# Optimization experiments

Measured on AMD Instinct MI355X. Metric: run time of the kernel, lower is better.

The kernel has to match this reference:

```python
import jax, jax.numpy as jnp
import numpy as np

B, S, D = 1, 2048, 1024
F = 1408            # expert intermediate dim
E = 16              # num experts
K = 2               # top_k
CAP_FACTOR = 1.25


def _mlp(h, wg, wu, wd):
    # DeepSeek-style gated MLP (SwiGLU, no bias)
    return (jax.nn.silu(h @ wg) * (h @ wu)) @ wd


def setup_inputs() -> dict:
    key = jax.random.key(0)
    ks = jax.random.split(key, 10)
    sd = 0.02
    return {
        "x": jax.random.normal(ks[0], (B, S, D), jnp.float32),
        "router_w": jax.random.normal(ks[1], (D, E), jnp.float32) * sd,
        "router_b": jnp.zeros((E,), jnp.float32),
        "w_gate": jax.random.normal(ks[2], (E, D, F), jnp.float32) * sd,
        "w_up": jax.random.normal(ks[3], (E, D, F), jnp.float32) * sd,
        "w_down": jax.random.normal(ks[4], (E, F, D), jnp.float32) * sd,
        "sw_gate": jax.random.normal(ks[5], (D, F), jnp.float32) * sd,
        "sw_up": jax.random.normal(ks[6], (D, F), jnp.float32) * sd,
        "sw_down": jax.random.normal(ks[7], (F, D), jnp.float32) * sd,
    }


def reference(x, router_w, router_b, w_gate, w_up, w_down, sw_gate, sw_up, sw_down):
    b, s, d = x.shape
    N = b * s
    NK = N * K
    C = int(np.ceil(CAP_FACTOR * NK / E))  # per-expert capacity

    x_tokens = x.reshape(N, d)

    # Router: softmax -> top-k -> renormalize
    logits = x_tokens @ router_w + router_b           # [N, E]
    probs = jax.nn.softmax(logits, axis=-1)
    vals, idx = jax.lax.top_k(probs, K)               # [N, K]
    vals = vals / (jnp.sum(vals, axis=-1, keepdims=True) + 1e-9)
    idx_flat = idx.reshape(NK)                        # int expert ids
    vals_flat = vals.reshape(NK)

    # Position within each expert's buffer = rank in flattened (token, k) order.
    # Same math as (cumsum(one_hot)*one_hot).sum(-1)-1 in the original.
    oh_e = jax.nn.one_hot(idx_flat, E, dtype=x.dtype)             # [NK, E] (small)
    pos = (jnp.cumsum(oh_e, axis=0) * oh_e).sum(axis=1) - 1       # [NK]
    within = (pos < C).astype(x.dtype)                            # capacity mask
    pos_c = jnp.clip(pos, 0, C - 1).astype(jnp.int32)

    # Dispatch: scatter tokens into per-expert buffers. Positions are unique
    # per expert, so scatter-add equals the dense one-hot einsum exactly.
    token_ids = jnp.arange(NK) // K
    x_pair = x_tokens[token_ids] * within[:, None]                # [NK, D]
    expert_inputs = jnp.zeros((E, C, d), x.dtype).at[idx_flat, pos_c].add(x_pair)

    # Grouped expert MLPs
    expert_outputs = jax.vmap(_mlp)(expert_inputs, w_gate, w_up, w_down)  # [E, C, D]

    # Combine: gather back and weight by renormalized router probs
    gathered = expert_outputs[idx_flat, pos_c] * (vals_flat * within)[:, None]
    output_tokens = gathered.reshape(N, K, d).sum(axis=1)         # [N, D]

    return x + _mlp(x, sw_gate, sw_up, sw_down) + output_tokens.reshape(b, s, d)
```

## Files before the change

### kernel.cpp

```cpp
#include <hip/hip_runtime.h>
#include <hip/hip_bf16.h>

#define TOKENS 2048
#define DIM    1024
#define FDIM   1408
#define NEXP   16
#define NK     (TOKENS * 2)
#define CAP    320
#define RPAD   384

typedef __attribute__((ext_vector_type(4))) float f32x4;
typedef __attribute__((ext_vector_type(8))) short s16x8;
typedef __attribute__((ext_vector_type(4))) short s16x4;

__device__ __forceinline__ short f2bf(float f) {
    unsigned int u = __float_as_uint(f);
    u += 0x7FFFu + ((u >> 16) & 1u);
    return (short)(u >> 16);
}
__device__ __forceinline__ float bf2f(short s) {
    return __uint_as_float(((unsigned int)(unsigned short)s) << 16);
}

#define GLDS16(gp, lp) __builtin_amdgcn_global_load_lds(                     \
    (const __attribute__((address_space(1))) unsigned int*)(gp),             \
    (__attribute__((address_space(3))) unsigned int*)(lp), 16, 0, 0)

struct GSeg {
    const short* A; long aStride; int aRpad;
    const short* B0; const short* B1; long bStride;
    short* Out; long oStride; int oRpad;
    const int* cnt; int Mb, Nb, N, K, nblocks;
};
struct WSeg { const float* in; short* out; int K, N, mats, nblocks; };

__device__ void wchunk_dev(const WSeg& W, int bid)
{
    const int pm  = W.nblocks / W.mats;
    const int mat = bid / pm, r = bid % pm;
    const int nbl = W.N >> 7;
    const int nb  = r % nbl, kb = r / nbl;
    const int t   = threadIdx.x;
    const int n   = nb * 128 + (t & 127);
    const int s0  = kb * 16 + (t >> 7);
    const float* in = W.in + (size_t)mat * W.K * W.N;
    short* out = W.out + (size_t)mat * W.K * W.N;
#pragma unroll
    for (int i = 0; i < 8; i++) {
        int s = s0 + i * 2;
        const float* src = in + (size_t)s * 8 * W.N + n;
        s16x8 o;
#pragma unroll
        for (int j = 0; j < 8; j++) o[j] = f2bf(src[(size_t)j * W.N]);
        *(s16x8*)(out + (size_t)s * W.N * 8 + (size_t)n * 8) = o;
    }
}

__device__ void router_dev(const float* __restrict__ x, const float* __restrict__ rw,
                           const float* __restrict__ rb, int* __restrict__ idx_flat,
                           float* __restrict__ vals_flat, int bid)
{
    __shared__ float lg[16][17];
    const int t  = threadIdx.x;
    const int tl = t >> 4;
    const int e  = t & 15;
    const int token = bid * 16 + tl;
    const float* xr = x + (size_t)token * DIM;

    float acc = 0.f;
    for (int d4 = 0; d4 < DIM / 4; d4++) {
        float4 xv = *(const float4*)(xr + d4 * 4);
        acc += xv.x * rw[(d4 * 4 + 0) * NEXP + e];
        acc += xv.y * rw[(d4 * 4 + 1) * NEXP + e];
        acc += xv.z * rw[(d4 * 4 + 2) * NEXP + e];
        acc += xv.w * rw[(d4 * 4 + 3) * NEXP + e];
    }
    lg[tl][e] = acc + rb[e];
    __syncthreads();

    if (t < 16) {
        float l[16];
#pragma unroll
        for (int j = 0; j < 16; j++) l[j] = lg[t][j];
        float m = l[0];
#pragma unroll
        for (int j = 1; j < 16; j++) m = fmaxf(m, l[j]);
        float p[16], den = 0.f;
#pragma unroll
        for (int j = 0; j < 16; j++) { p[j] = __expf(l[j] - m); den += p[j]; }
        int i1 = -1; float b1 = -1e30f;
#pragma unroll
        for (int j = 0; j < 16; j++) if (p[j] > b1) { b1 = p[j]; i1 = j; }
        int i2 = -1; float b2 = -1e30f;
#pragma unroll
        for (int j = 0; j < 16; j++) if (j != i1 && p[j] > b2) { b2 = p[j]; i2 = j; }
        float v1 = b1 / den, v2 = b2 / den;
        float s = v1 + v2 + 1e-9f;
        int tok = bid * 16 + t;
        idx_flat[tok * 2 + 0] = i1;
        idx_flat[tok * 2 + 1] = i2;
        vals_flat[tok * 2 + 0] = v1 / s;
        vals_flat[tok * 2 + 1] = v2 / s;
    }
}

__device__ void xconv_dev(const float* __restrict__ x, short* __restrict__ xb, int bid)
{
    const int token = bid * 2 + (threadIdx.x >> 7);
    const int c = threadIdx.x & 127;
    const float* src = x + (size_t)token * DIM + c * 8;
    float4 v0 = *(const float4*)(src);
    float4 v1 = *(const float4*)(src + 4);
    s16x8 o;
    o[0] = f2bf(v0.x); o[1] = f2bf(v0.y); o[2] = f2bf(v0.z); o[3] = f2bf(v0.w);
    o[4] = f2bf(v1.x); o[5] = f2bf(v1.y); o[6] = f2bf(v1.z); o[7] = f2bf(v1.w);
    *(s16x8*)(xb + (size_t)c * (TOKENS * 8) + (size_t)token * 8) = o;
}

__global__ __launch_bounds__(256) void prep_kernel(
    WSeg w0, WSeg w1, WSeg w2, WSeg w3,
    const float* __restrict__ x, const float* __restrict__ rw,
    const float* __restrict__ rb, int* __restrict__ idx_flat,
    float* __restrict__ vals, short* __restrict__ xb)
{
    int bid = blockIdx.x;
    if (bid < w0.nblocks) { wchunk_dev(w0, bid); return; }
    bid -= w0.nblocks;
    if (bid < w1.nblocks) { wchunk_dev(w1, bid); return; }
    bid -= w1.nblocks;
    if (bid < w2.nblocks) { wchunk_dev(w2, bid); return; }
    bid -= w2.nblocks;
    if (bid < w3.nblocks) { wchunk_dev(w3, bid); return; }
    bid -= w3.nblocks;
    if (bid < TOKENS / 16) { router_dev(x, rw, rb, idx_flat, vals, bid); return; }
    bid -= TOKENS / 16;
    xconv_dev(x, xb, bid);
}

__global__ void scan_kernel(const int* __restrict__ idx_flat,
                            const float* __restrict__ vals,
                            int* __restrict__ dst, float* __restrict__ wgt,
                            int* __restrict__ cnt)
{
    const int lane = threadIdx.x;
    int base[16];
#pragma unroll
    for (int e = 0; e < 16; e++) base[e] = 0;

    for (int c = 0; c < NK / 64; c++) {
        int i = c * 64 + lane;
        int e = idx_flat[i];
        unsigned long long m[16];
#pragma unroll
        for (int ee = 0; ee < 16; ee++) m[ee] = __ballot(e == ee);
        unsigned long long mym = 0ULL; int myb = 0;
#pragma unroll
        for (int ee = 0; ee < 16; ee++) {
            bool sel = (e == ee);
            mym = sel ? m[ee] : mym;
            myb = sel ? base[ee] : myb;
        }
        int pos = myb + (int)__popcll(mym & ((1ULL << lane) - 1ULL));
        bool within = pos < CAP;
        dst[i] = within ? (e * RPAD + pos) : -1;
        wgt[i] = within ? vals[i] : 0.f;
#pragma unroll
        for (int ee = 0; ee < 16; ee++) base[ee] += (int)__popcll(m[ee]);
    }
    if (lane < 16) cnt[lane] = base[lane] < CAP ? base[lane] : CAP;
}

__global__ __launch_bounds__(256) void scatter_kernel(
    const float* __restrict__ x, const int* __restrict__ dst,
    const int* __restrict__ idx_flat, short* __restrict__ ex)
{
    const int i = blockIdx.x * 2 + (threadIdx.x >> 7);
    const int d0 = dst[i];
    if (d0 < 0) return;
    const int e = idx_flat[i];
    const int pos = d0 - e * RPAD;
    const int token = i >> 1;
    const int c = threadIdx.x & 127;
    const float* src = x + (size_t)token * DIM + c * 8;
    float4 v0 = *(const float4*)(src);
    float4 v1 = *(const float4*)(src + 4);
    s16x8 o;
    o[0] = f2bf(v0.x); o[1] = f2bf(v0.y); o[2] = f2bf(v0.z); o[3] = f2bf(v0.w);
    o[4] = f2bf(v1.x); o[5] = f2bf(v1.y); o[6] = f2bf(v1.z); o[7] = f2bf(v1.w);
    *(s16x8*)(ex + (size_t)e * (DIM * RPAD) + (size_t)c * (RPAD * 8) +
              (size_t)pos * 8) = o;
}

template <int NMAT>
__device__ void gemm_dev(const GSeg& S, int bid)
{
    constexpr int BUFS = 4096 * (1 + NMAT);
    __shared__ short lds[2 * BUFS];

    const int cpx = S.nblocks >> 3;
    const int lid = (bid & 7) * cpx + (bid >> 3);
    const int mb  = lid % S.Mb;
    const int t1  = lid / S.Mb;
    const int nb  = t1 % S.Nb;
    const int g   = t1 / S.Nb;
    const int m0 = mb * 128, n0 = nb * 128;
    if (S.cnt != nullptr && m0 >= S.cnt[g]) return;

    const int tid = threadIdx.x, lane = tid & 63, w = tid >> 6;
    const int wr = w >> 1, wc = w & 1, ln = lane & 15, kg = lane >> 4;

    const int N = S.N, K = S.K;
    const short* Ag  = S.A  + (size_t)g * S.aStride + (size_t)m0 * 8;
    const short* Bg0 = S.B0 + (size_t)g * S.bStride + (size_t)n0 * 8;
    const short* Bg1 = nullptr;
    if constexpr (NMAT == 2) Bg1 = S.B1 + (size_t)g * S.bStride + (size_t)n0 * 8;

    const size_t aR8 = (size_t)S.aRpad * 8;
    const size_t n8  = (size_t)N * 8;

    const int srow = tid & 127, sslab = tid >> 7;
    const short* aS0 = Ag  + sslab * aR8 + srow * 8;
    const short* aS1 = Ag  + (2 + sslab) * aR8 + srow * 8;
    const short* bS00 = Bg0 + sslab * n8 + srow * 8;
    const short* bS01 = Bg0 + (2 + sslab) * n8 + srow * 8;
    const short* bS10 = nullptr, *bS11 = nullptr;
    if constexpr (NMAT == 2) {
        bS10 = Bg1 + sslab * n8 + srow * 8;
        bS11 = Bg1 + (2 + sslab) * n8 + srow * 8;
    }

    const int dA0 = w * 512, dA1 = 2048 + w * 512;

    auto STG = [&](int buf, int ks) {
        const size_t ka = (size_t)ks * 4 * aR8;
        const size_t kb = (size_t)ks * 4 * n8;
        short* base = lds + buf * BUFS;
        GLDS16(aS0 + ka,  base + dA0);
        GLDS16(aS1 + ka,  base + dA1);
        GLDS16(bS00 + kb, base + 4096 + dA0);
        GLDS16(bS01 + kb, base + 4096 + dA1);
        if constexpr (NMAT == 2) {
            GLDS16(bS10 + kb, base + 8192 + dA0);
            GLDS16(bS11 + kb, base + 8192 + dA1);
        }
    };

    const int aO = kg * 1024 + (wr * 64 + ln) * 8;
    const int bO = kg * 1024 + (wc * 64 + ln) * 8;

    f32x4 acc[NMAT][4][4] = {};

    const int nt = K / 32;
    STG(0, 0); STG(1, 1);
    int cur = 0;
    for (int ks = 0; ks < nt; ks++) {
        if (ks + 1 < nt) {
            if constexpr (NMAT == 2) asm volatile("s_waitcnt vmcnt(6)" ::: "memory");
            else                     asm volatile("s_waitcnt vmcnt(4)" ::: "memory");
        } else {
            asm volatile("s_waitcnt vmcnt(0)" ::: "memory");
        }
        __builtin_amdgcn_s_barrier();
        __builtin_amdgcn_sched_barrier(0);

        const short* base = lds + cur * BUFS;
        s16x8 af[4];
#pragma unroll
        for (int m = 0; m < 4; m++)
            af[m] = *(const s16x8*)(base + aO + m * 128);
        s16x8 bf[NMAT][4];
#pragma unroll
        for (int mat = 0; mat < NMAT; mat++)
#pragma unroll
            for (int nf = 0; nf < 4; nf++)
                bf[mat][nf] = *(const s16x8*)(base + 4096 + mat * 4096 + bO + nf * 128);

        __builtin_amdgcn_s_setprio(1);
#pragma unroll
        for (int nf = 0; nf < 4; nf++)
#pragma unroll
            for (int m = 0; m < 4; m++)
#pragma unroll
                for (int mat = 0; mat < NMAT; mat++)
                    acc[mat][m][nf] = __builtin_amdgcn_mfma_f32_16x16x32_bf16(
                        af[m], bf[mat][nf], acc[mat][m][nf], 0, 0, 0);
        __builtin_amdgcn_s_setprio(0);
        __builtin_amdgcn_sched_barrier(0);
        __builtin_amdgcn_s_barrier();

        if (ks + 2 < nt) STG(cur, ks + 2);
        cur ^= 1;
    }

#pragma unroll
    for (int m = 0; m < 4; m++) {
#pragma unroll
        for (int nf = 0; nf < 4; nf++) {
            const int row = m0 + wr * 64 + m * 16 + kg * 4;
            const int col = n0 + wc * 64 + nf * 16 + ln;
#pragma unroll
            for (int j = 0; j < 4; j++) {
                if constexpr (NMAT == 2) {
                    float gv = acc[0][m][nf][j];
                    float uv = acc[1][m][nf][j];
                    float v = gv / (1.f + __expf(-gv)) * uv;
                    S.Out[(size_t)g * S.oStride + (size_t)(col >> 3) * (S.oRpad * 8) +
                          (size_t)(row + j) * 8 + (col & 7)] = f2bf(v);
                } else {
                    S.Out[(size_t)g * S.oStride + (size_t)(row + j) * N + col] =
                        f2bf(acc[0][m][nf][j]);
                }
            }
        }
    }
}

__global__ __launch_bounds__(256, 2) void gateup_kernel(GSeg s0, GSeg s1,
                                                        WSeg w0, WSeg w1)
{
    int bid = blockIdx.x;
    if (bid < s0.nblocks) { gemm_dev<2>(s0, bid); return; }
    bid -= s0.nblocks;
    if (bid < s1.nblocks) { gemm_dev<2>(s1, bid); return; }
    bid -= s1.nblocks;
    if (bid < w0.nblocks) { wchunk_dev(w0, bid); return; }
    bid -= w0.nblocks;
    wchunk_dev(w1, bid);
}

__global__ __launch_bounds__(256, 2) void down_kernel(GSeg s0, GSeg s1)
{
    int bid = blockIdx.x;
    if (bid < s0.nblocks) { gemm_dev<1>(s0, bid); return; }
    bid -= s0.nblocks;
    gemm_dev<1>(s1, bid);
}

__global__ __launch_bounds__(256) void combine_kernel(
    const float* __restrict__ x, const short* __restrict__ shout,
    const short* __restrict__ eout, const int* __restrict__ dst,
    const float* __restrict__ wgt, float* __restrict__ out)
{
    const int t = blockIdx.x;
    const int d = threadIdx.x * 4;
    size_t o = (size_t)t * DIM + d;
    float4 xv = *(const float4*)(x + o);
    s16x4 sv = *(const s16x4*)(shout + o);
    float r0 = xv.x + bf2f(sv[0]);
    float r1 = xv.y + bf2f(sv[1]);
    float r2 = xv.z + bf2f(sv[2]);
    float r3 = xv.w + bf2f(sv[3]);
#pragma unroll
    for (int k = 0; k < 2; k++) {
        int di = dst[t * 2 + k];
        if (di >= 0) {
            float wv = wgt[t * 2 + k];
            s16x4 ev = *(const s16x4*)(eout + (size_t)di * DIM + d);
            r0 += wv * bf2f(ev[0]);
            r1 += wv * bf2f(ev[1]);
            r2 += wv * bf2f(ev[2]);
            r3 += wv * bf2f(ev[3]);
        }
    }
    float4 rv = {r0, r1, r2, r3};
    *(float4*)(out + o) = rv;
}

extern "C" void kernel_launch(void* const* d_in, const int* in_sizes, int n_in,
                              void* d_out, int out_size, void* d_ws, size_t ws_size,
                              hipStream_t stream)
{
    const float* x   = (const float*)d_in[0];
    const float* rw  = (const float*)d_in[1];
    const float* rb  = (const float*)d_in[2];
    const float* wg  = (const float*)d_in[3];
    const float* wu  = (const float*)d_in[4];
    const float* wd  = (const float*)d_in[5];
    const float* swg = (const float*)d_in[6];
    const float* swu = (const float*)d_in[7];
    const float* swd = (const float*)d_in[8];
    float* out = (float*)d_out;

    char* wp = (char*)d_ws;
    auto alloc = [&](size_t b) { char* p = wp; wp += (b + 255) & ~(size_t)255; return p; };
    int*   idx_flat = (int*)alloc((size_t)NK * 4);
    float* vals     = (float*)alloc((size_t)NK * 4);
    int*   dst      = (int*)alloc((size_t)NK * 4);
    float* wgt      = (float*)alloc((size_t)NK * 4);
    int*   cnt      = (int*)alloc(64);
    short* xb       = (short*)alloc((size_t)TOKENS * DIM * 2);
    short* ex       = (short*)alloc((size_t)NEXP * RPAD * DIM * 2);
    short* acte     = (short*)alloc((size_t)NEXP * RPAD * FDIM * 2);
    short* acts     = (short*)alloc((size_t)TOKENS * FDIM * 2);
    short* eout     = (short*)alloc((size_t)NEXP * RPAD * DIM * 2);
    short* shout    = (short*)alloc((size_t)TOKENS * DIM * 2);
    short* wgC      = (short*)alloc((size_t)NEXP * DIM * FDIM * 2);
    short* wuC      = (short*)alloc((size_t)NEXP * DIM * FDIM * 2);
    short* wdC      = (short*)alloc((size_t)NEXP * DIM * FDIM * 2);
    short* swgC     = (short*)alloc((size_t)DIM * FDIM * 2);
    short* swuC     = (short*)alloc((size_t)DIM * FDIM * 2);
    short* swdC     = (short*)alloc((size_t)DIM * FDIM * 2);

    WSeg Wg  = {wg,  wgC,  DIM,  FDIM, NEXP, 11 * 8 * NEXP};
    WSeg Wu  = {wu,  wuC,  DIM,  FDIM, NEXP, 11 * 8 * NEXP};
    WSeg Wsg = {swg, swgC, DIM,  FDIM, 1,    11 * 8};
    WSeg Wsu = {swu, swuC, DIM,  FDIM, 1,    11 * 8};
    WSeg Wd  = {wd,  wdC,  FDIM, DIM,  NEXP, 8 * 11 * NEXP};
    WSeg Wsd = {swd, swdC, FDIM, DIM,  1,    8 * 11};

    const int prep_blocks = Wg.nblocks + Wu.nblocks + Wsg.nblocks + Wsu.nblocks
                          + TOKENS / 16 + TOKENS / 2;
    prep_kernel<<<prep_blocks, 256, 0, stream>>>(Wg, Wu, Wsg, Wsu,
                                                 x, rw, rb, idx_flat, vals, xb);
    scan_kernel<<<1, 64, 0, stream>>>(idx_flat, vals, dst, wgt, cnt);
    scatter_kernel<<<NK / 2, 256, 0, stream>>>(x, dst, idx_flat, ex);

    GSeg segGE = {ex, (long)RPAD * DIM, RPAD, wgC, wuC, (long)DIM * FDIM,
                  acte, (long)RPAD * FDIM, RPAD, cnt, 3, 11, FDIM, DIM, 3 * 11 * NEXP};
    GSeg segGS = {xb, 0L, TOKENS, swgC, swuC, 0L,
                  acts, 0L, TOKENS, nullptr, 16, 11, FDIM, DIM, 16 * 11};
    gateup_kernel<<<segGE.nblocks + segGS.nblocks + Wd.nblocks + Wsd.nblocks,
                    256, 0, stream>>>(segGE, segGS, Wd, Wsd);

    GSeg segDE = {acte, (long)RPAD * FDIM, RPAD, wdC, nullptr, (long)DIM * FDIM,
                  eout, (long)RPAD * DIM, 0, cnt, 3, 8, DIM, FDIM, 3 * 8 * NEXP};
    GSeg segDS = {acts, 0L, TOKENS, swdC, nullptr, 0L,
                  shout, 0L, 0, nullptr, 16, 8, DIM, FDIM, 16 * 8};
    down_kernel<<<segDE.nblocks + segDS.nblocks, 256, 0, stream>>>(segDE, segDS);

    combine_kernel<<<TOKENS, 256, 0, stream>>>(x, shout, eout, dst, wgt, out);
}
```

Baseline: 250.5 us.

## Split router out, fuse weight conversion with scatter, widen weight-convert loads

Moves the router into its own small kernel that runs before the scan. The weight bf16 conversion, x conversion and token scatter are merged into one mid kernel that runs after the scan, so the scatter launch disappears and the scan no longer waits on the bulky weight conversion. The weight conversion is also rewritten so each block handles one 8-row slab with float2 loads across the row, which gives wider coalesced reads. The cost is that the router and scan now run serially ahead of the large conversion work instead of overlapping with it.

```diff
diff --git a/kernel.cpp b/kernel.cpp
--- a/kernel.cpp
+++ b/kernel.cpp
@@ -36,35 +36,38 @@
 
 __device__ void wchunk_dev(const WSeg& W, int bid)
 {
-    const int pm  = W.nblocks / W.mats;
-    const int mat = bid / pm, r = bid % pm;
-    const int nbl = W.N >> 7;
-    const int nb  = r % nbl, kb = r / nbl;
-    const int t   = threadIdx.x;
-    const int n   = nb * 128 + (t & 127);
-    const int s0  = kb * 16 + (t >> 7);
-    const float* in = W.in + (size_t)mat * W.K * W.N;
-    short* out = W.out + (size_t)mat * W.K * W.N;
-#pragma unroll
-    for (int i = 0; i < 8; i++) {
-        int s = s0 + i * 2;
-        const float* src = in + (size_t)s * 8 * W.N + n;
-        s16x8 o;
-#pragma unroll
-        for (int j = 0; j < 8; j++) o[j] = f2bf(src[(size_t)j * W.N]);
-        *(s16x8*)(out + (size_t)s * W.N * 8 + (size_t)n * 8) = o;
-    }
-}
-
-__device__ void router_dev(const float* __restrict__ x, const float* __restrict__ rw,
-                           const float* __restrict__ rb, int* __restrict__ idx_flat,
-                           float* __restrict__ vals_flat, int bid)
+    const int spm = W.K >> 3;
+    const int mat = bid / spm, s = bid % spm;
+    const float* in  = W.in  + (size_t)mat * W.K * W.N + (size_t)s * 8 * W.N;
+    short* out = W.out + (size_t)mat * W.K * W.N + (size_t)s * W.N * 8;
+    const int t = threadIdx.x;
+    const int iters = (W.N + 511) >> 9;
+    for (int it = 0; it < iters; it++) {
+        const int n = it * 512 + 2 * t;
+        if (n >= W.N) break;
+        const float* src = in + n;
+        s16x8 o0, o1;
+#pragma unroll
+        for (int j = 0; j < 8; j++) {
+            float2 v = *(const float2*)(src + (size_t)j * W.N);
+            o0[j] = f2bf(v.x);
+            o1[j] = f2bf(v.y);
+        }
+        *(s16x8*)(out + (size_t)n * 8)     = o0;
+        *(s16x8*)(out + (size_t)n * 8 + 8) = o1;
+    }
+}
+
+__global__ __launch_bounds__(256) void router_kernel(
+    const float* __restrict__ x, const float* __restrict__ rw,
+    const float* __restrict__ rb, int* __restrict__ idx_flat,
+    float* __restrict__ vals_flat)
 {
     __shared__ float lg[16][17];
     const int t  = threadIdx.x;
     const int tl = t >> 4;
     const int e  = t & 15;
-    const int token = bid * 16 + tl;
+    const int token = blockIdx.x * 16 + tl;
     const float* xr = x + (size_t)token * DIM;
 
     float acc = 0.f;
@@ -96,12 +99,45 @@
         for (int j = 0; j < 16; j++) if (j != i1 && p[j] > b2) { b2 = p[j]; i2 = j; }
         float v1 = b1 / den, v2 = b2 / den;
         float s = v1 + v2 + 1e-9f;
-        int tok = bid * 16 + t;
+        int tok = blockIdx.x * 16 + t;
         idx_flat[tok * 2 + 0] = i1;
         idx_flat[tok * 2 + 1] = i2;
         vals_flat[tok * 2 + 0] = v1 / s;
         vals_flat[tok * 2 + 1] = v2 / s;
     }
+}
+
+__global__ void scan_kernel(const int* __restrict__ idx_flat,
+                            const float* __restrict__ vals,
+                            int* __restrict__ dst, float* __restrict__ wgt,
+                            int* __restrict__ cnt)
+{
+    const int lane = threadIdx.x;
+    int base[16];
+#pragma unroll
+    for (int e = 0; e < 16; e++) base[e] = 0;
+
+    for (int c = 0; c < NK / 64; c++) {
+        int i = c * 64 + lane;
+        int e = idx_flat[i];
+        unsigned long long m[16];
+#pragma unroll
+        for (int ee = 0; ee < 16; ee++) m[ee] = __ballot(e == ee);
+        unsigned long long mym = 0ULL; int myb = 0;
+#pragma unroll
+        for (int ee = 0; ee < 16; ee++) {
+            bool sel = (e == ee);
+            mym = sel ? m[ee] : mym;
+            myb = sel ? base[ee] : myb;
+        }
+        int pos = myb + (int)__popcll(mym & ((1ULL << lane) - 1ULL));
+        bool within = pos < CAP;
+        dst[i] = within ? (e * RPAD + pos) : -1;
+        wgt[i] = within ? vals[i] : 0.f;
+#pragma unroll
+        for (int ee = 0; ee < 16; ee++) base[ee] += (int)__popcll(m[ee]);
+    }
+    if (lane < 16) cnt[lane] = base[lane] < CAP ? base[lane] : CAP;
 }
 
 __device__ void xconv_dev(const float* __restrict__ x, short* __restrict__ xb, int bid)
@@ -117,64 +153,11 @@
     *(s16x8*)(xb + (size_t)c * (TOKENS * 8) + (size_t)token * 8) = o;
 }
 
-__global__ __launch_bounds__(256) void prep_kernel(
-    WSeg w0, WSeg w1, WSeg w2, WSeg w3,
-    const float* __restrict__ x, const float* __restrict__ rw,
-    const float* __restrict__ rb, int* __restrict__ idx_flat,
-    float* __restrict__ vals, short* __restrict__ xb)
-{
-    int bid = blockIdx.x;
-    if (bid < w0.nblocks) { wchunk_dev(w0, bid); return; }
-    bid -= w0.nblocks;
-    if (bid < w1.nblocks) { wchunk_dev(w1, bid); return; }
-    bid -= w1.nblocks;
-    if (bid < w2.nblocks) { wchunk_dev(w2, bid); return; }
-    bid -= w2.nblocks;
-    if (bid < w3.nblocks) { wchunk_dev(w3, bid); return; }
-    bid -= w3.nblocks;
-    if (bid < TOKENS / 16) { router_dev(x, rw, rb, idx_flat, vals, bid); return; }
-    bid -= TOKENS / 16;
-    xconv_dev(x, xb, bid);
-}
-
-__global__ void scan_kernel(const int* __restrict__ idx_flat,
-                            const float* __restrict__ vals,
-                            int* __restrict__ dst, float* __restrict__ wgt,
-                            int* __restrict__ cnt)
-{
-    const int lane = threadIdx.x;
-    int base[16];
-#pragma unroll
-    for (int e = 0; e < 16; e++) base[e] = 0;
-
-    for (int c = 0; c < NK / 64; c++) {
-        int i = c * 64 + lane;
-        int e = idx_flat[i];
-        unsigned long long m[16];
-#pragma unroll
-        for (int ee = 0; ee < 16; ee++) m[ee] = __ballot(e == ee);
-        unsigned long long mym = 0ULL; int myb = 0;
-#pragma unroll
-        for (int ee = 0; ee < 16; ee++) {
-            bool sel = (e == ee);
-            mym = sel ? m[ee] : mym;
-            myb = sel ? base[ee] : myb;
-        }
-        int pos = myb + (int)__popcll(mym & ((1ULL << lane) - 1ULL));
-        bool within = pos < CAP;
-        dst[i] = within ? (e * RPAD + pos) : -1;
-        wgt[i] = within ? vals[i] : 0.f;
-#pragma unroll
-        for (int ee = 0; ee < 16; ee++) base[ee] += (int)__popcll(m[ee]);
-    }
-    if (lane < 16) cnt[lane] = base[lane] < CAP ? base[lane] : CAP;
-}
-
-__global__ __launch_bounds__(256) void scatter_kernel(
-    const float* __restrict__ x, const int* __restrict__ dst,
-    const int* __restrict__ idx_flat, short* __restrict__ ex)
-{
-    const int i = blockIdx.x * 2 + (threadIdx.x >> 7);
+__device__ void scatter_dev(const float* __restrict__ x, const int* __restrict__ dst,
+                            const int* __restrict__ idx_flat, short* __restrict__ ex,
+                            int bid)
+{
+    const int i = bid * 2 + (threadIdx.x >> 7);
     const int d0 = dst[i];
     if (d0 < 0) return;
     const int e = idx_flat[i];
@@ -189,6 +172,26 @@
     o[4] = f2bf(v1.x); o[5] = f2bf(v1.y); o[6] = f2bf(v1.z); o[7] = f2bf(v1.w);
     *(s16x8*)(ex + (size_t)e * (DIM * RPAD) + (size_t)c * (RPAD * 8) +
               (size_t)pos * 8) = o;
+}
+
+__global__ __launch_bounds__(256) void mid_kernel(
+    WSeg w0, WSeg w1, WSeg w2, WSeg w3,
+    const float* __restrict__ x, short* __restrict__ xb,
+    const int* __restrict__ dst, const int* __restrict__ idx_flat,
+    short* __restrict__ ex)
+{
+    int bid = blockIdx.x;
+    if (bid < w0.nblocks) { wchunk_dev(w0, bid); return; }
+    bid -= w0.nblocks;
+    if (bid < w1.nblocks) { wchunk_dev(w1, bid); return; }
+    bid -= w1.nblocks;
+    if (bid < w2.nblocks) { wchunk_dev(w2, bid); return; }
+    bid -= w2.nblocks;
+    if (bid < w3.nblocks) { wchunk_dev(w3, bid); return; }
+    bid -= w3.nblocks;
+    if (bid < TOKENS / 2) { xconv_dev(x, xb, bid); return; }
+    bid -= TOKENS / 2;
+    scatter_dev(x, dst, idx_flat, ex, bid);
 }
 
 template <int NMAT>
@@ -401,19 +404,20 @@
     short* swuC     = (short*)alloc((size_t)DIM * FDIM * 2);
     short* swdC     = (short*)alloc((size_t)DIM * FDIM * 2);
 
-    WSeg Wg  = {wg,  wgC,  DIM,  FDIM, NEXP, 11 * 8 * NEXP};
-    WSeg Wu  = {wu,  wuC,  DIM,  FDIM, NEXP, 11 * 8 * NEXP};
-    WSeg Wsg = {swg, swgC, DIM,  FDIM, 1,    11 * 8};
-    WSeg Wsu = {swu, swuC, DIM,  FDIM, 1,    11 * 8};
-    WSeg Wd  = {wd,  wdC,  FDIM, DIM,  NEXP, 8 * 11 * NEXP};
-    WSeg Wsd = {swd, swdC, FDIM, DIM,  1,    8 * 11};
-
-    const int prep_blocks = Wg.nblocks + Wu.nblocks + Wsg.nblocks + Wsu.nblocks
-                          + TOKENS / 16 + TOKENS / 2;
-    prep_kernel<<<prep_blocks, 256, 0, stream>>>(Wg, Wu, Wsg, Wsu,
-                                                 x, rw, rb, idx_flat, vals, xb);
+    WSeg Wg  = {wg,  wgC,  DIM,  FDIM, NEXP, NEXP * (DIM / 8)};
+    WSeg Wu  = {wu,  wuC,  DIM,  FDIM, NEXP, NEXP * (DIM / 8)};
+    WSeg Wsg = {swg, swgC, DIM,  FDIM, 1,    DIM / 8};
+    WSeg Wsu = {swu, swuC, DIM,  FDIM, 1,    DIM / 8};
+    WSeg Wd  = {wd,  wdC,  FDIM, DIM,  NEXP, NEXP * (FDIM / 8)};
+    WSeg Wsd = {swd, swdC, FDIM, DIM,  1,    FDIM / 8};
+
+    router_kernel<<<TOKENS / 16, 256, 0, stream>>>(x, rw, rb, idx_flat, vals);
     scan_kernel<<<1, 64, 0, stream>>>(idx_flat, vals, dst, wgt, cnt);
-    scatter_kernel<<<NK / 2, 256, 0, stream>>>(x, dst, idx_flat, ex);
+
+    const int mid_blocks = Wg.nblocks + Wu.nblocks + Wsg.nblocks + Wsu.nblocks
+                         + TOKENS / 2 + NK / 2;
+    mid_kernel<<<mid_blocks, 256, 0, stream>>>(Wg, Wu, Wsg, Wsu,
+                                               x, xb, dst, idx_flat, ex);
 
     GSeg segGE = {ex, (long)RPAD * DIM, RPAD, wgC, wuC, (long)DIM * FDIM,
                   acte, (long)RPAD * FDIM, RPAD, cnt, 3, 11, FDIM, DIM, 3 * 11 * NEXP};
```

Result: no change. 249.5 us (-0.4%).
